# Kernel tuning notes

Hardware: AMD Instinct MI355X
Metric: run time of the kernel (lower is better)

The kernel has to match this reference:

```python
import jax, jax.numpy as jnp
import numpy as np

NUM_OUT_POINTS = 8192  # init kwarg num_out_points


def setup_inputs() -> dict:
    key = jax.random.key(0)
    B, C, N = 32, 64, 65536
    x = jax.random.normal(key, (B, C, N), dtype=jnp.float32)
    return {"x": x}


def reference(x):
    # x: [B, C, N]. For each batch element draw a random permutation of the
    # N points and keep the first NUM_OUT_POINTS indices, then gather.
    B, C, N = x.shape
    keys = jax.random.split(jax.random.key(1), B)
    # idx: [B, K] int32, each row a prefix of an independent permutation of N
    idx = jax.vmap(lambda k: jax.random.permutation(k, N)[:NUM_OUT_POINTS])(keys)
    idx = idx.astype(jnp.int32)
    # gather along point axis: y[b, c, k] = x[b, c, idx[b, k]]
    y = jnp.take_along_axis(x, idx[:, None, :].astype(jnp.int64), axis=2)
    return y
```

## Files before the change

kernel.cpp:

```cpp
#include <hip/hip_runtime.h>
#include <stdint.h>

#define B_SZ 32
#define C_SZ 64
#define N_SZ 65536
#define K_SZ 8192
#define BCAP 384
#define NHEAD 48
#define JCAP 80

__device__ __forceinline__ uint32_t rotl32(uint32_t v, int r) {
  return (v << r) | (v >> (32 - r));
}

__device__ __forceinline__ void threefry2x32(uint32_t k0, uint32_t k1,
                                             uint32_t x0, uint32_t x1,
                                             uint32_t& o0, uint32_t& o1) {
  const uint32_t ks2 = k0 ^ k1 ^ 0x1BD11BDAu;
  x0 += k0; x1 += k1;
#define TF_R(r) { x0 += x1; x1 = rotl32(x1, (r)); x1 ^= x0; }
  TF_R(13) TF_R(15) TF_R(26) TF_R(6)   x0 += k1;  x1 += ks2 + 1u;
  TF_R(17) TF_R(29) TF_R(16) TF_R(24)  x0 += ks2; x1 += k0  + 2u;
  TF_R(13) TF_R(15) TF_R(26) TF_R(6)   x0 += k0;  x1 += k1  + 3u;
  TF_R(17) TF_R(29) TF_R(16) TF_R(24)  x0 += k1;  x1 += ks2 + 4u;
  TF_R(13) TF_R(15) TF_R(26) TF_R(6)   x0 += ks2; x1 += k0  + 5u;
#undef TF_R
  o0 = x0; o1 = x1;
}

__device__ __forceinline__ void subkey_for_round(int b, int round,
                                                 uint32_t& sk0, uint32_t& sk1) {
  uint32_t c0, c1;
  threefry2x32(0u, 1u, 0u, (uint32_t)b, c0, c1);
  for (int r = 0; r < round; ++r) {
    uint32_t n0, n1;
    threefry2x32(c0, c1, 0u, 0u, n0, n1);
    c0 = n0; c1 = n1;
  }
  threefry2x32(c0, c1, 0u, 1u, sk0, sk1);
}

__device__ __forceinline__ uint32_t block_excl_scan(uint32_t h, int t,
                                                    uint32_t* __restrict__ wsum) {
  const int lane = t & 63, w = t >> 6;
  uint32_t inc = h;
#pragma unroll
  for (int off = 1; off < 64; off <<= 1) {
    const uint32_t y = __shfl_up(inc, off, 64);
    if (lane >= off) inc += y;
  }
  if (lane == 63) wsum[w] = inc;
  __syncthreads();
  uint32_t woff = 0;
#pragma unroll
  for (int w2 = 0; w2 < 4; ++w2)
    if (w2 < w) woff += wsum[w2];
  return woff + inc - h;
}

__global__ __launch_bounds__(256) void zero_cnt(uint32_t* __restrict__ z) {
  z[blockIdx.x * 256 + threadIdx.x] = 0;
}

__global__ __launch_bounds__(256) void gen_scatter1(uint64_t* __restrict__ BVfix,
                                                    uint32_t* __restrict__ cnt1) {
  __shared__ uint32_t lcnt[256];
  __shared__ uint32_t gb[256];
  const int t = threadIdx.x, chunk = blockIdx.x, b = blockIdx.y;
  lcnt[t] = 0; __syncthreads();
  uint32_t sk0, sk1;
  subkey_for_round(b, 0, sk0, sk1);
  uint64_t v[16]; uint32_t r[16], dg[16];
  const int base = chunk * 4096;
#pragma unroll
  for (int e = 0; e < 16; ++e) {
    const int i = base + e * 256 + t;
    uint32_t o0, o1;
    threefry2x32(sk0, sk1, 0u, (uint32_t)i, o0, o1);
    const uint32_t bits = o0 ^ o1;
    v[e] = ((uint64_t)bits << 16) | (uint64_t)i;
    dg[e] = bits >> 24;
    r[e] = atomicAdd(&lcnt[dg[e]], 1u);
  }
  __syncthreads();
  if (lcnt[t]) gb[t] = atomicAdd(&cnt1[b * 256 + t], lcnt[t]);
  __syncthreads();
#pragma unroll
  for (int e = 0; e < 16; ++e) {
    const uint32_t slot = gb[dg[e]] + r[e];
    if (slot < BCAP)
      BVfix[((size_t)(b * 256 + dg[e])) * BCAP + slot] = v[e];
  }
}

__global__ __launch_bounds__(256) void prefix1(const uint32_t* __restrict__ cnt1,
                                               uint32_t* __restrict__ baseArr,
                                               uint32_t* __restrict__ cnt2) {
  __shared__ uint32_t wsum[4];
  const int b = blockIdx.x, d = threadIdx.x;
  cnt2[b * 256 + d] = 0;
  uint32_t h = cnt1[b * 256 + d];
  if (h > BCAP) h = BCAP;
  const uint32_t excl = block_excl_scan(h, d, wsum);
  baseArr[b * 257 + d] = excl;
  if (d == 255) baseArr[b * 257 + 256] = excl + h;
}

__global__ __launch_bounds__(256) void rank_sort1(const uint64_t* __restrict__ BVfix,
                                                  const uint32_t* __restrict__ cnt1,
                                                  const uint32_t* __restrict__ baseArr,
                                                  uint16_t* __restrict__ S1v) {
  __shared__ uint32_t sub[BCAP];
  __shared__ uint16_t dg[BCAP];
  __shared__ uint16_t idxt[BCAP];
  __shared__ uint32_t hist[256];
  __shared__ uint32_t cur[256];
  __shared__ uint32_t base2[257];
  __shared__ uint32_t wsum[4];
  const int t = threadIdx.x, u = blockIdx.x, b = blockIdx.y;
  uint32_t n = cnt1[b * 256 + u];
  if (n > BCAP) n = BCAP;
  const uint64_t* __restrict__ g = BVfix + ((size_t)(b * 256 + u)) * BCAP;
  const uint32_t base = baseArr[b * 257 + u];

  hist[t] = 0; __syncthreads();
  uint64_t rec[2] = {0, 0};
#pragma unroll
  for (int w = 0; w < 2; ++w) {
    const int e = t + w * 256;
    if (e < (int)n) {
      rec[w] = g[e];
      const uint32_t key = (uint32_t)(rec[w] >> 16);
      const uint32_t d = (key >> 16) & 0xFFu;
      sub[e] = ((key & 0xFFFFu) << 16) | (uint32_t)(rec[w] & 0xFFFFull);
      dg[e] = (uint16_t)d;
      atomicAdd(&hist[d], 1u);
    }
  }
  __syncthreads();
  const uint32_t h = hist[t];
  const uint32_t excl = block_excl_scan(h, t, wsum);
  base2[t] = excl;
  cur[t] = excl;
  if (t == 255) base2[256] = excl + h;
  __syncthreads();
#pragma unroll
  for (int w = 0; w < 2; ++w) {
    const int e = t + w * 256;
    if (e < (int)n) idxt[atomicAdd(&cur[dg[e]], 1u)] = (uint16_t)e;
  }
  __syncthreads();
  uint16_t* __restrict__ out = S1v + (size_t)b * N_SZ + base;
#pragma unroll
  for (int w = 0; w < 2; ++w) {
    const int e = t + w * 256;
    if (e < (int)n) {
      const uint32_t d = dg[e], s = sub[e];
      const uint32_t lo = base2[d], hi = base2[d + 1];
      uint32_t r = 0;
      for (uint32_t i = lo; i < hi; ++i) r += (sub[idxt[i]] < s) ? 1u : 0u;
      out[lo + r] = (uint16_t)(rec[w] & 0xFFFFull);
    }
  }
}

__global__ __launch_bounds__(256) void gen_scatter2(const uint16_t* __restrict__ S1v,
                                                    uint64_t* __restrict__ CVfix,
                                                    uint32_t* __restrict__ cnt2) {
  __shared__ uint32_t lcnt[256];
  __shared__ uint32_t gb[256];
  const int t = threadIdx.x, chunk = blockIdx.x, b = blockIdx.y;
  lcnt[t] = 0; __syncthreads();
  uint32_t sk0, sk1;
  subkey_for_round(b, 1, sk0, sk1);
  const uint16_t* __restrict__ s1 = S1v + (size_t)b * N_SZ;
  uint64_t v[16]; uint32_t r[16], dg[16];
  const int base = chunk * 4096;
#pragma unroll
  for (int e = 0; e < 16; ++e) {
    const int i = base + e * 256 + t;
    uint32_t o0, o1;
    threefry2x32(sk0, sk1, 0u, (uint32_t)i, o0, o1);
    const uint32_t bits = o0 ^ o1;
    dg[e] = bits >> 24;
    if (dg[e] < NHEAD) {
      v[e] = ((uint64_t)bits << 32) | ((uint64_t)(uint32_t)i << 16) | (uint64_t)s1[i];
      r[e] = atomicAdd(&lcnt[dg[e]], 1u);
    }
  }
  __syncthreads();
  if (t < NHEAD && lcnt[t]) gb[t] = atomicAdd(&cnt2[b * 256 + t], lcnt[t]);
  __syncthreads();
#pragma unroll
  for (int e = 0; e < 16; ++e) {
    if (dg[e] < NHEAD) {
      const uint32_t slot = gb[dg[e]] + r[e];
      if (slot < BCAP)
        CVfix[((size_t)(b * NHEAD + dg[e])) * BCAP + slot] = v[e];
    }
  }
}

__global__ __launch_bounds__(256) void prefix2(const uint32_t* __restrict__ cnt2,
                                               uint32_t* __restrict__ baseArr2,
                                               uint32_t* __restrict__ jcnt) {
  __shared__ uint32_t wsum[4];
  const int b = blockIdx.x, d = threadIdx.x;
  jcnt[b * 256 + d] = 0;
  uint32_t h = 0;
  if (d < NHEAD) { h = cnt2[b * 256 + d]; if (h > BCAP) h = BCAP; }
  const uint32_t excl = block_excl_scan(h, d, wsum);
  if (d < NHEAD) baseArr2[b * NHEAD + d] = excl;
}

__global__ __launch_bounds__(256) void finalize_rank(const uint64_t* __restrict__ CVfix,
                                                     const uint32_t* __restrict__ cnt2,
                                                     const uint32_t* __restrict__ baseArr2,
                                                     uint32_t* __restrict__ jcnt,
                                                     uint32_t* __restrict__ jb) {
  __shared__ uint32_t sub[BCAP];
  __shared__ uint16_t dg[BCAP];
  __shared__ uint16_t idxt[BCAP];
  __shared__ uint32_t hist[256];
  __shared__ uint32_t cur[256];
  __shared__ uint32_t base2[257];
  __shared__ uint32_t wsum[4];
  const int t = threadIdx.x, u = blockIdx.x, b = blockIdx.y;
  const uint32_t base = baseArr2[b * NHEAD + u];
  if (base >= K_SZ) return;
  uint32_t n = cnt2[b * 256 + u];
  if (n > BCAP) n = BCAP;
  const uint64_t* __restrict__ g = CVfix + ((size_t)(b * NHEAD + u)) * BCAP;

  hist[t] = 0; __syncthreads();
  uint64_t rec[2] = {0, 0};
#pragma unroll
  for (int w = 0; w < 2; ++w) {
    const int e = t + w * 256;
    if (e < (int)n) {
      rec[w] = g[e];
      const uint32_t key = (uint32_t)(rec[w] >> 32);
      const uint32_t d = (key >> 16) & 0xFFu;
      sub[e] = ((key & 0xFFFFu) << 16) | (uint32_t)((rec[w] >> 16) & 0xFFFFull);
      dg[e] = (uint16_t)d;
      atomicAdd(&hist[d], 1u);
    }
  }
  __syncthreads();
  const uint32_t h = hist[t];
  const uint32_t excl = block_excl_scan(h, t, wsum);
  base2[t] = excl;
  cur[t] = excl;
  if (t == 255) base2[256] = excl + h;
  __syncthreads();
#pragma unroll
  for (int w = 0; w < 2; ++w) {
    const int e = t + w * 256;
    if (e < (int)n) idxt[atomicAdd(&cur[dg[e]], 1u)] = (uint16_t)e;
  }
  __syncthreads();
#pragma unroll
  for (int w = 0; w < 2; ++w) {
    const int e = t + w * 256;
    if (e < (int)n) {
      const uint32_t d = dg[e], s = sub[e];
      const uint32_t lo = base2[d], hi = base2[d + 1];
      uint32_t r = 0;
      for (uint32_t i = lo; i < hi; ++i) r += (sub[idxt[i]] < s) ? 1u : 0u;
      const uint32_t q = base + lo + r;
      if (q < K_SZ) {
        const uint32_t j = (uint32_t)(rec[w] & 0xFFFFull);
        const uint32_t slot = atomicAdd(&jcnt[b * 256 + (j >> 8)], 1u);
        if (slot < JCAP)
          jb[((size_t)b * 256 + (j >> 8)) * JCAP + slot] = (j << 16) | q;
      }
    }
  }
}

__global__ __launch_bounds__(256) void compact_pairs(const uint32_t* __restrict__ jcnt,
                                                     const uint32_t* __restrict__ jb,
                                                     uint32_t* __restrict__ sp) {
  __shared__ uint32_t wsum[4];
  const int b = blockIdx.x, t = threadIdx.x;
  uint32_t c = jcnt[b * 256 + t];
  if (c > JCAP) c = JCAP;
  const uint32_t base = block_excl_scan(c, t, wsum);
  const uint32_t* __restrict__ src = jb + ((size_t)b * 256 + t) * JCAP;
  uint32_t* __restrict__ dst = sp + (size_t)b * K_SZ + base;
  for (uint32_t i = 0; i < c; ++i) dst[i] = src[i];
}

__global__ __launch_bounds__(256) void gather_staged(const float* __restrict__ x,
                                                     const uint32_t* __restrict__ sp,
                                                     float* __restrict__ y) {
  __shared__ float row[K_SZ];
  const int t = threadIdx.x, c = blockIdx.x, b = blockIdx.y;
  const uint32_t* __restrict__ spb = sp + (size_t)b * K_SZ;
  const float* __restrict__ xr = x + ((size_t)b * C_SZ + c) * N_SZ;
#pragma unroll 8
  for (int w = 0; w < 32; ++w) {
    const uint32_t p = spb[w * 256 + t];
    row[p & 0xFFFFu] = xr[p >> 16];
  }
  __syncthreads();
  float4* __restrict__ yr4 = (float4*)(y + ((size_t)b * C_SZ + c) * K_SZ);
  const float4* __restrict__ r4 = (const float4*)row;
#pragma unroll
  for (int w = 0; w < 8; ++w) yr4[w * 256 + t] = r4[w * 256 + t];
}

extern "C" void kernel_launch(void* const* d_in, const int* in_sizes, int n_in,
                              void* d_out, int out_size, void* d_ws, size_t ws_size,
                              hipStream_t stream) {
  (void)in_sizes; (void)n_in; (void)out_size; (void)ws_size;
  const float* x = (const float*)d_in[0];
  float* y = (float*)d_out;

  char* base = (char*)d_out;
  uint64_t* BVfix = (uint64_t*)base;
  uint64_t* CVfix = (uint64_t*)(base + (26u << 20));
  uint16_t* S1v   = (uint16_t*)(base + (31u << 20));
  uint32_t* baseArr  = (uint32_t*)(base + (36u << 20));
  uint32_t* baseArr2 = (uint32_t*)(base + (37u << 20));
  uint32_t* cnt1 = (uint32_t*)d_ws;
  uint32_t* cnt2 = (uint32_t*)((char*)d_ws + (32u << 10));
  uint32_t* jcnt = (uint32_t*)((char*)d_ws + (64u << 10));
  uint32_t* jb   = (uint32_t*)((char*)d_ws + (128u << 10));
  uint32_t* sp   = (uint32_t*)((char*)d_ws + (4u << 20));

  const dim3 blk(256);
  const dim3 ggen(16, B_SZ);

  zero_cnt<<<dim3(B_SZ), blk, 0, stream>>>(cnt1);
  gen_scatter1<<<ggen, blk, 0, stream>>>(BVfix, cnt1);
  prefix1<<<dim3(B_SZ), blk, 0, stream>>>(cnt1, baseArr, cnt2);
  rank_sort1<<<dim3(256, B_SZ), blk, 0, stream>>>(BVfix, cnt1, baseArr, S1v);
  gen_scatter2<<<ggen, blk, 0, stream>>>(S1v, CVfix, cnt2);
  prefix2<<<dim3(B_SZ), blk, 0, stream>>>(cnt2, baseArr2, jcnt);
  finalize_rank<<<dim3(NHEAD, B_SZ), blk, 0, stream>>>(CVfix, cnt2, baseArr2, jcnt, jb);
  compact_pairs<<<dim3(B_SZ), blk, 0, stream>>>(jcnt, jb, sp);
  gather_staged<<<dim3(C_SZ, B_SZ), blk, 0, stream>>>(x, sp, y);
}
```

Baseline: 193.4 us.

## Fold prefix-scan kernels into consumers and parallelize pair compaction

Drops the two standalone prefix kernels. Each rank_sort1 and finalize_rank block now recomputes the per-batch exclusive scan over bucket counts itself and picks out its own base and count. zero_cnt is widened to 96 blocks so it also clears cnt2 and jcnt, which the prefix kernels used to reset. compact_pairs now builds a shared byte map from output slot to source bucket, so all threads copy in a coalesced, strided pattern instead of each thread copying its own bucket serially. The cost is redundant scan work in every block and two fewer launches in a pipeline that is mostly launches and serialization.

New measurement: 187.0 us. 1.03x faster.

```diff
diff --git a/kernel.cpp b/kernel.cpp
--- a/kernel.cpp
+++ b/kernel.cpp
@@ -93,22 +93,8 @@
   }
 }
 
-__global__ __launch_bounds__(256) void prefix1(const uint32_t* __restrict__ cnt1,
-                                               uint32_t* __restrict__ baseArr,
-                                               uint32_t* __restrict__ cnt2) {
-  __shared__ uint32_t wsum[4];
-  const int b = blockIdx.x, d = threadIdx.x;
-  cnt2[b * 256 + d] = 0;
-  uint32_t h = cnt1[b * 256 + d];
-  if (h > BCAP) h = BCAP;
-  const uint32_t excl = block_excl_scan(h, d, wsum);
-  baseArr[b * 257 + d] = excl;
-  if (d == 255) baseArr[b * 257 + 256] = excl + h;
-}
-
 __global__ __launch_bounds__(256) void rank_sort1(const uint64_t* __restrict__ BVfix,
                                                   const uint32_t* __restrict__ cnt1,
-                                                  const uint32_t* __restrict__ baseArr,
                                                   uint16_t* __restrict__ S1v) {
   __shared__ uint32_t sub[BCAP];
   __shared__ uint16_t dg[BCAP];
@@ -117,11 +103,19 @@
   __shared__ uint32_t cur[256];
   __shared__ uint32_t base2[257];
   __shared__ uint32_t wsum[4];
+  __shared__ uint32_t sh_bn[2];
   const int t = threadIdx.x, u = blockIdx.x, b = blockIdx.y;
-  uint32_t n = cnt1[b * 256 + u];
-  if (n > BCAP) n = BCAP;
+
+  {
+    uint32_t hh = cnt1[b * 256 + t];
+    if (hh > BCAP) hh = BCAP;
+    const uint32_t excl0 = block_excl_scan(hh, t, wsum);
+    if (t == u) { sh_bn[0] = excl0; sh_bn[1] = hh; }
+  }
+  __syncthreads();
+  const uint32_t base = sh_bn[0];
+  const uint32_t n = sh_bn[1];
   const uint64_t* __restrict__ g = BVfix + ((size_t)(b * 256 + u)) * BCAP;
-  const uint32_t base = baseArr[b * 257 + u];
 
   hist[t] = 0; __syncthreads();
   uint64_t rec[2] = {0, 0};
@@ -201,21 +195,8 @@
   }
 }
 
-__global__ __launch_bounds__(256) void prefix2(const uint32_t* __restrict__ cnt2,
-                                               uint32_t* __restrict__ baseArr2,
-                                               uint32_t* __restrict__ jcnt) {
-  __shared__ uint32_t wsum[4];
-  const int b = blockIdx.x, d = threadIdx.x;
-  jcnt[b * 256 + d] = 0;
-  uint32_t h = 0;
-  if (d < NHEAD) { h = cnt2[b * 256 + d]; if (h > BCAP) h = BCAP; }
-  const uint32_t excl = block_excl_scan(h, d, wsum);
-  if (d < NHEAD) baseArr2[b * NHEAD + d] = excl;
-}
-
 __global__ __launch_bounds__(256) void finalize_rank(const uint64_t* __restrict__ CVfix,
                                                      const uint32_t* __restrict__ cnt2,
-                                                     const uint32_t* __restrict__ baseArr2,
                                                      uint32_t* __restrict__ jcnt,
                                                      uint32_t* __restrict__ jb) {
   __shared__ uint32_t sub[BCAP];
@@ -225,11 +206,19 @@
   __shared__ uint32_t cur[256];
   __shared__ uint32_t base2[257];
   __shared__ uint32_t wsum[4];
+  __shared__ uint32_t sh_bn[2];
   const int t = threadIdx.x, u = blockIdx.x, b = blockIdx.y;
-  const uint32_t base = baseArr2[b * NHEAD + u];
+
+  {
+    uint32_t hh = 0;
+    if (t < NHEAD) { hh = cnt2[b * 256 + t]; if (hh > BCAP) hh = BCAP; }
+    const uint32_t excl0 = block_excl_scan(hh, t, wsum);
+    if (t == u) { sh_bn[0] = excl0; sh_bn[1] = hh; }
+  }
+  __syncthreads();
+  const uint32_t base = sh_bn[0];
   if (base >= K_SZ) return;
-  uint32_t n = cnt2[b * 256 + u];
-  if (n > BCAP) n = BCAP;
+  const uint32_t n = sh_bn[1];
   const uint64_t* __restrict__ g = CVfix + ((size_t)(b * NHEAD + u)) * BCAP;
 
   hist[t] = 0; __syncthreads();
@@ -281,14 +270,24 @@
 __global__ __launch_bounds__(256) void compact_pairs(const uint32_t* __restrict__ jcnt,
                                                      const uint32_t* __restrict__ jb,
                                                      uint32_t* __restrict__ sp) {
+  __shared__ uint32_t bases[256];
+  __shared__ uint8_t map8[K_SZ];
   __shared__ uint32_t wsum[4];
   const int b = blockIdx.x, t = threadIdx.x;
   uint32_t c = jcnt[b * 256 + t];
   if (c > JCAP) c = JCAP;
-  const uint32_t base = block_excl_scan(c, t, wsum);
-  const uint32_t* __restrict__ src = jb + ((size_t)b * 256 + t) * JCAP;
-  uint32_t* __restrict__ dst = sp + (size_t)b * K_SZ + base;
-  for (uint32_t i = 0; i < c; ++i) dst[i] = src[i];
+  const uint32_t excl = block_excl_scan(c, t, wsum);
+  bases[t] = excl;
+  for (uint32_t i = 0; i < c; ++i)
+    if (excl + i < K_SZ) map8[excl + i] = (uint8_t)t;
+  __syncthreads();
+  const uint32_t* __restrict__ jbb = jb + (size_t)b * 256 * JCAP;
+  uint32_t* __restrict__ dst = sp + (size_t)b * K_SZ;
+#pragma unroll 8
+  for (int k = t; k < K_SZ; k += 256) {
+    const uint32_t d = map8[k];
+    dst[k] = jbb[d * JCAP + (k - bases[d])];
+  }
 }
 
 __global__ __launch_bounds__(256) void gather_staged(const float* __restrict__ x,
@@ -321,8 +320,6 @@
   uint64_t* BVfix = (uint64_t*)base;
   uint64_t* CVfix = (uint64_t*)(base + (26u << 20));
   uint16_t* S1v   = (uint16_t*)(base + (31u << 20));
-  uint32_t* baseArr  = (uint32_t*)(base + (36u << 20));
-  uint32_t* baseArr2 = (uint32_t*)(base + (37u << 20));
   uint32_t* cnt1 = (uint32_t*)d_ws;
   uint32_t* cnt2 = (uint32_t*)((char*)d_ws + (32u << 10));
   uint32_t* jcnt = (uint32_t*)((char*)d_ws + (64u << 10));
@@ -332,13 +329,11 @@
   const dim3 blk(256);
   const dim3 ggen(16, B_SZ);
 
-  zero_cnt<<<dim3(B_SZ), blk, 0, stream>>>(cnt1);
+  zero_cnt<<<dim3(96), blk, 0, stream>>>(cnt1);
   gen_scatter1<<<ggen, blk, 0, stream>>>(BVfix, cnt1);
-  prefix1<<<dim3(B_SZ), blk, 0, stream>>>(cnt1, baseArr, cnt2);
-  rank_sort1<<<dim3(256, B_SZ), blk, 0, stream>>>(BVfix, cnt1, baseArr, S1v);
+  rank_sort1<<<dim3(256, B_SZ), blk, 0, stream>>>(BVfix, cnt1, S1v);
   gen_scatter2<<<ggen, blk, 0, stream>>>(S1v, CVfix, cnt2);
-  prefix2<<<dim3(B_SZ), blk, 0, stream>>>(cnt2, baseArr2, jcnt);
-  finalize_rank<<<dim3(NHEAD, B_SZ), blk, 0, stream>>>(CVfix, cnt2, baseArr2, jcnt, jb);
+  finalize_rank<<<dim3(NHEAD, B_SZ), blk, 0, stream>>>(CVfix, cnt2, jcnt, jb);
   compact_pairs<<<dim3(B_SZ), blk, 0, stream>>>(jcnt, jb, sp);
   gather_staged<<<dim3(C_SZ, B_SZ), blk, 0, stream>>>(x, sp, y);
 }
```
